# Kernel optimization log

Hardware: AMD Instinct MI355X
Metric: run time of the kernel (lower is better)

Reference implementation:

```python
import jax, jax.numpy as jnp
import numpy as np

EPS_LN = 1e-3
EPS_ATTN = 1e-8
D = 256       # slot_dim == feature_dim (required by the torch code)
H_MLP = 512
NUM_ITERS = 3  # step == 0 -> num_initial_iterations
SCALE = D ** (-0.5)


def _layernorm(x, g, b):
    m = jnp.mean(x, axis=-1, keepdims=True)
    v = jnp.mean(jnp.square(x - m), axis=-1, keepdims=True)
    return (x - m) * jax.lax.rsqrt(v + EPS_LN) * g + b


def _gru_cell(x, h, W_ih, b_ih, W_hh, b_hh):
    # torch GRUCell: W_ih [3D, D], W_hh [3D, D], gate order r, z, n
    gi = x @ W_ih.T + b_ih
    gh = h @ W_hh.T + b_hh
    i_r, i_z, i_n = jnp.split(gi, 3, axis=-1)
    h_r, h_z, h_n = jnp.split(gh, 3, axis=-1)
    r = jax.nn.sigmoid(i_r + h_r)
    z = jax.nn.sigmoid(i_z + h_z)
    n = jnp.tanh(i_n + r * h_n)
    return (1.0 - z) * n + z * h


def setup_inputs() -> dict:
    key = jax.random.key(0)
    ks = jax.random.split(key, 16)
    s = 0.02
    inp = {
        "inputs": jax.random.normal(ks[0], (32, 4096, D), jnp.float32),
        "slots": jax.random.normal(ks[1], (32, 8, D), jnp.float32),
        "step": 0,
        "ln_in_g": jnp.ones((D,), jnp.float32),
        "ln_in_b": jnp.zeros((D,), jnp.float32),
        "ln_slot_g": jnp.ones((D,), jnp.float32),
        "ln_slot_b": jnp.zeros((D,), jnp.float32),
        "ln_mlp_g": jnp.ones((D,), jnp.float32),
        "ln_mlp_b": jnp.zeros((D,), jnp.float32),
        "Wq": jax.random.normal(ks[2], (D, D), jnp.float32) * s,
        "bq": jnp.zeros((D,), jnp.float32),
        "Wk": jax.random.normal(ks[3], (D, D), jnp.float32) * s,
        "bk": jnp.zeros((D,), jnp.float32),
        "Wv": jax.random.normal(ks[4], (D, D), jnp.float32) * s,
        "bv": jnp.zeros((D,), jnp.float32),
        "W_ih": jax.random.normal(ks[5], (3 * D, D), jnp.float32) * s,
        "b_ih": jnp.zeros((3 * D,), jnp.float32),
        "W_hh": jax.random.normal(ks[6], (3 * D, D), jnp.float32) * s,
        "b_hh": jnp.zeros((3 * D,), jnp.float32),
        "W1": jax.random.normal(ks[7], (H_MLP, D), jnp.float32) * s,
        "b1": jnp.zeros((H_MLP,), jnp.float32),
        "W2": jax.random.normal(ks[8], (D, H_MLP), jnp.float32) * s,
        "b2": jnp.zeros((D,), jnp.float32),
    }
    return inp


def reference(inputs, slots, step, ln_in_g, ln_in_b, ln_slot_g, ln_slot_b,
              ln_mlp_g, ln_mlp_b, Wq, bq, Wk, bk, Wv, bv,
              W_ih, b_ih, W_hh, b_hh, W1, b1, W2, b2):
    B = inputs.shape[0]
    x = _layernorm(inputs, ln_in_g, ln_in_b)          # [B, N, D]
    k = x @ Wk.T + bk                                  # [B, N, D]
    v = x @ Wv.T + bv                                  # [B, N, D]
    num_iters = NUM_ITERS  # step == 0 -> num_initial_iterations
    for _ in range(num_iters):
        slots_prev = slots
        s_n = _layernorm(slots, ln_slot_g, ln_slot_b)  # [B, S, D]
        q = s_n @ Wq.T + bq                            # [B, S, D]
        dots = jnp.einsum('bid,bjd->bij', q, k) * SCALE  # [B, S, N]
        attn = jax.nn.softmax(dots, axis=1) + EPS_ATTN   # competitive over slots
        attn = attn / jnp.sum(attn, axis=-1, keepdims=True)
        updates = jnp.einsum('bij,bjd->bid', attn, v)  # [B, S, D]
        slots = _gru_cell(updates.reshape(-1, D), slots_prev.reshape(-1, D),
                          W_ih, b_ih, W_hh, b_hh).reshape(B, -1, D)
        mlp = jax.nn.relu(_layernorm(slots, ln_mlp_g, ln_mlp_b) @ W1.T + b1) @ W2.T + b2
        slots = slots + mlp
    return slots
```

## Files before the change

### kernel.cpp

```cpp
#include <hip/hip_runtime.h>
#include <stdint.h>


typedef __attribute__((ext_vector_type(8))) short bf16x8;
typedef __attribute__((ext_vector_type(4))) float f32x4;

__device__ __forceinline__ float bf2f_lo(uint32_t u) {
    union { uint32_t u; float f; } v; v.u = u << 16; return v.f;
}
__device__ __forceinline__ float bf2f_hi(uint32_t u) {
    union { uint32_t u; float f; } v; v.u = u & 0xffff0000u; return v.f;
}
__device__ __forceinline__ unsigned short f2bf(float f) {
    union { float f; uint32_t u; } v; v.f = f;
    return (unsigned short)((v.u + 0x7fffu + ((v.u >> 16) & 1u)) >> 16);
}
__device__ __forceinline__ float sigf(float x) { return 1.0f / (1.0f + __expf(-x)); }
__device__ __forceinline__ void gld_lds16(const void* g, void* l) {
    __builtin_amdgcn_global_load_lds(
        (__attribute__((address_space(1))) unsigned int*)g,
        (__attribute__((address_space(3))) unsigned int*)l, 16, 0, 0);
}

__global__ __launch_bounds__(256) void prep_k(
    const float* __restrict__ in, const float* __restrict__ ln_in_g,
    const float* __restrict__ ln_in_b, unsigned short* __restrict__ xbf,
    const float* __restrict__ Wk, const float* __restrict__ Wv,
    const float* __restrict__ W_ih, const float* __restrict__ W_hh,
    const float* __restrict__ W1, const float* __restrict__ W2,
    const float* __restrict__ bk, const float* __restrict__ bv,
    const float* __restrict__ b_ih, const float* __restrict__ b_hh,
    unsigned short* __restrict__ Wkv, unsigned short* __restrict__ Wg,
    unsigned short* __restrict__ W1b, unsigned short* __restrict__ W2b,
    unsigned short* __restrict__ Wqb,
    float* __restrict__ bkv, float* __restrict__ bg,
    const float* __restrict__ slots_in, const float* __restrict__ g_slot,
    const float* __restrict__ b_slot, const float* __restrict__ Wq,
    const float* __restrict__ bq, unsigned short* __restrict__ qbuf) {
    __shared__ __align__(16) char smem[16384];
    int bid = blockIdx.x, t = threadIdx.x;
    int wave = t >> 6, lane = t & 63;

    if (bid >= 3360) {
        float (*xs)[256] = (float(*)[256])smem;
        size_t rb = (size_t)(bid - 3360) * 16 + wave * 4;
        const float* gsrc = in + rb * 256;
#pragma unroll
        for (int i = 0; i < 4; ++i)
            gld_lds16(gsrc + i * 256 + lane * 4, &xs[wave * 4 + i][0]);
        __syncthreads();

        float4 g4 = *(const float4*)(ln_in_g + lane * 4);
        float4 b4 = *(const float4*)(ln_in_b + lane * 4);
#pragma unroll
        for (int p = 0; p < 2; ++p) {
            float4 x0 = *(const float4*)&xs[wave * 4 + p * 2 + 0][lane * 4];
            float4 x1 = *(const float4*)&xs[wave * 4 + p * 2 + 1][lane * 4];
            float s0 = x0.x + x0.y + x0.z + x0.w;
            float q0 = x0.x * x0.x + x0.y * x0.y + x0.z * x0.z + x0.w * x0.w;
            float s1 = x1.x + x1.y + x1.z + x1.w;
            float q1 = x1.x * x1.x + x1.y * x1.y + x1.z * x1.z + x1.w * x1.w;
#pragma unroll
            for (int off = 32; off > 0; off >>= 1) {
                s0 += __shfl_xor(s0, off, 64);  q0 += __shfl_xor(q0, off, 64);
                s1 += __shfl_xor(s1, off, 64);  q1 += __shfl_xor(q1, off, 64);
            }
            float m0 = s0 * (1.0f / 256.0f);
            float r0 = rsqrtf(q0 * (1.0f / 256.0f) - m0 * m0 + 1e-3f);
            float m1 = s1 * (1.0f / 256.0f);
            float r1 = rsqrtf(q1 * (1.0f / 256.0f) - m1 * m1 + 1e-3f);
            uint2 o0, o1;
            o0.x = (uint32_t)f2bf((x0.x - m0) * r0 * g4.x + b4.x) |
                   ((uint32_t)f2bf((x0.y - m0) * r0 * g4.y + b4.y) << 16);
            o0.y = (uint32_t)f2bf((x0.z - m0) * r0 * g4.z + b4.z) |
                   ((uint32_t)f2bf((x0.w - m0) * r0 * g4.w + b4.w) << 16);
            o1.x = (uint32_t)f2bf((x1.x - m1) * r1 * g4.x + b4.x) |
                   ((uint32_t)f2bf((x1.y - m1) * r1 * g4.y + b4.y) << 16);
            o1.y = (uint32_t)f2bf((x1.z - m1) * r1 * g4.z + b4.z) |
                   ((uint32_t)f2bf((x1.w - m1) * r1 * g4.w + b4.w) << 16);
            *(uint2*)(xbf + (rb + p * 2 + 0) * 256 + lane * 4) = o0;
            *(uint2*)(xbf + (rb + p * 2 + 1) * 256 + lane * 4) = o1;
        }
        return;
    }
    if (bid >= 32) {
        int i = (bid - 32) * 256 + t;
        if (i < 131072) {
            float v = (i < 65536) ? Wk[i] : Wv[i - 65536];
            Wkv[i] = f2bf(v);
        } else if (i < 524288) {
            int j = i - 131072;
            Wg[j] = f2bf(j < 196608 ? W_ih[j] : W_hh[j - 196608]);
        } else if (i < 655360) W1b[i - 524288] = f2bf(W1[i - 524288]);
        else if (i < 786432)   W2b[i - 655360] = f2bf(W2[i - 655360]);
        else                   Wqb[i - 786432] = f2bf(Wq[i - 786432]);
        if (i < 512)           bkv[i] = (i < 256 ? bk[i] : bv[i - 256]);
        else if (i < 2048)   { int j = i - 512; bg[j] = (j < 768 ? b_ih[j] : b_hh[j - 768]); }
        return;
    }
    int b = bid;
    unsigned short* A1 = (unsigned short*)smem;
    {
        float4 g4 = *(const float4*)(g_slot + lane * 4);
        float4 b4 = *(const float4*)(b_slot + lane * 4);
#pragma unroll
        for (int rep = 0; rep < 2; ++rep) {
            int s = wave * 2 + rep;
            float4 x = *(const float4*)(slots_in + (size_t)b * 2048 + s * 256 + lane * 4);
            float sm = x.x + x.y + x.z + x.w;
            float sq = x.x * x.x + x.y * x.y + x.z * x.z + x.w * x.w;
#pragma unroll
            for (int off = 32; off > 0; off >>= 1) {
                sm += __shfl_xor(sm, off, 64);
                sq += __shfl_xor(sq, off, 64);
            }
            float mean = sm * (1.0f / 256.0f);
            float rstd = rsqrtf(sq * (1.0f / 256.0f) - mean * mean + 1e-3f);
            uint2 o;
            o.x = (uint32_t)f2bf((x.x - mean) * rstd * g4.x + b4.x) |
                  ((uint32_t)f2bf((x.y - mean) * rstd * g4.y + b4.y) << 16);
            o.y = (uint32_t)f2bf((x.z - mean) * rstd * g4.z + b4.z) |
                  ((uint32_t)f2bf((x.w - mean) * rstd * g4.w + b4.w) << 16);
            *(uint2*)&A1[s * 264 + lane * 4] = o;
        }
    }
    __syncthreads();
    {
        bf16x8 af[8];
#pragma unroll
        for (int ks = 0; ks < 8; ++ks)
            af[ks] = *(const bf16x8*)&A1[(lane & 15) * 264 + ks * 32 + (lane >> 4) * 8];
#pragma unroll
        for (int nt = 0; nt < 4; ++nt) {
            int n0 = (wave * 4 + nt) * 16;
            f32x4 a = {0.f, 0.f, 0.f, 0.f};
#pragma unroll
            for (int ks = 0; ks < 8; ++ks) {
                const float* wp = Wq + (size_t)(n0 + (lane & 15)) * 256 +
                                  ks * 32 + (lane >> 4) * 8;
                float4 wa = *(const float4*)wp;
                float4 wb = *(const float4*)(wp + 4);
                bf16x8 bfr;
                bfr[0] = (short)f2bf(wa.x); bfr[1] = (short)f2bf(wa.y);
                bfr[2] = (short)f2bf(wa.z); bfr[3] = (short)f2bf(wa.w);
                bfr[4] = (short)f2bf(wb.x); bfr[5] = (short)f2bf(wb.y);
                bfr[6] = (short)f2bf(wb.z); bfr[7] = (short)f2bf(wb.w);
                a = __builtin_amdgcn_mfma_f32_16x16x32_bf16(af[ks], bfr, a, 0, 0, 0);
            }
            int col = n0 + (lane & 15);
            float bs = bq[col];
#pragma unroll
            for (int r = 0; r < 4; ++r) {
                int row = (lane >> 4) * 4 + r;
                if (row < 8)
                    qbuf[((size_t)b * 8 + row) * 256 + col] = f2bf(a[r] + bs);
            }
        }
    }
}

__global__ __launch_bounds__(256) void gemm_kv(const unsigned short* __restrict__ X,
                                               const unsigned short* __restrict__ W,
                                               const float* __restrict__ bkv,
                                               unsigned short* __restrict__ Ko,
                                               unsigned short* __restrict__ Vo) {
    __shared__ __align__(16) unsigned short As[128 * 64];
    __shared__ __align__(16) unsigned short Bs[128 * 64];
    int t = threadIdx.x, wave = t >> 6, lane = t & 63;
    int wr = wave >> 1, wc = wave & 1;
    int bid = blockIdx.x;
    int m0 = (((bid >> 5) << 3) | (bid & 7)) * 128;
    int j0 = ((bid >> 3) & 3) * 128;

    int rsub = lane >> 3;
    int sblk = (lane & 7) ^ rsub;

    f32x4 acc[4][4];
#pragma unroll
    for (int i = 0; i < 4; ++i)
#pragma unroll
        for (int j = 0; j < 4; ++j)
#pragma unroll
            for (int r = 0; r < 4; ++r) acc[i][j][r] = 0.f;

    for (int kb = 0; kb < 4; ++kb) {
        int k0 = kb * 64;
#pragma unroll
        for (int i = 0; i < 4; ++i) {
            int rbase = wave * 32 + i * 8;
            gld_lds16(X + (size_t)(m0 + rbase + rsub) * 256 + k0 + sblk * 8,
                      &As[rbase * 64]);
            gld_lds16(W + (size_t)(j0 + rbase + rsub) * 256 + k0 + sblk * 8,
                      &Bs[rbase * 64]);
        }
        __syncthreads();
#pragma unroll
        for (int kk = 0; kk < 64; kk += 32) {
            int koff = kk + (lane >> 4) * 8;
            int cl = koff >> 3;
            bf16x8 af[4], bf[4];
#pragma unroll
            for (int ti = 0; ti < 4; ++ti) {
                int r = wr * 64 + ti * 16 + (lane & 15);
                af[ti] = *(const bf16x8*)&As[r * 64 + ((cl ^ (r & 7)) << 3)];
            }
#pragma unroll
            for (int tj = 0; tj < 4; ++tj) {
                int c = wc * 64 + tj * 16 + (lane & 15);
                bf[tj] = *(const bf16x8*)&Bs[c * 64 + ((cl ^ (c & 7)) << 3)];
            }
#pragma unroll
            for (int ti = 0; ti < 4; ++ti)
#pragma unroll
                for (int tj = 0; tj < 4; ++tj)
                    acc[ti][tj] = __builtin_amdgcn_mfma_f32_16x16x32_bf16(
                        af[ti], bf[tj], acc[ti][tj], 0, 0, 0);
        }
        __syncthreads();
    }
    bool isK = (j0 < 256);
    unsigned short* base = isK ? Ko : Vo;
#pragma unroll
    for (int ti = 0; ti < 4; ++ti)
#pragma unroll
        for (int tj = 0; tj < 4; ++tj) {
            int col = j0 + wc * 64 + tj * 16 + (lane & 15);
            float bias = bkv[col];
            int outc = col & 255;
#pragma unroll
            for (int r = 0; r < 4; ++r) {
                int row = m0 + wr * 64 + ti * 16 + (lane >> 4) * 4 + r;
                base[(size_t)row * 256 + outc] = f2bf(acc[ti][tj][r] + bias);
            }
        }
}

__global__ __launch_bounds__(256) void attn_fused(
    const unsigned short* __restrict__ qb, const unsigned short* __restrict__ K,
    const unsigned short* __restrict__ V,
    float* __restrict__ upd_part, float* __restrict__ sums_part) {
    __shared__ __align__(16) unsigned short qs[8 * 264];
    __shared__ __align__(16) float atf[8 * 256];
    __shared__ __align__(16) float pr[4][8 * 256];
    __shared__ float ssum[8];
    int b = blockIdx.x, ch = blockIdx.y, t = threadIdx.x;
    int wave = t >> 6, lane = t & 63;

    *(uint4*)&qs[(t >> 5) * 264 + (t & 31) * 8] = ((const uint4*)(qb + (size_t)b * 2048))[t];
    if (t < 8) ssum[t] = 0.f;
    __syncthreads();

    {
        bf16x8 af[8];
#pragma unroll
        for (int ks = 0; ks < 8; ++ks)
            af[ks] = *(const bf16x8*)&qs[(lane & 7) * 264 + ks * 32 + (lane >> 4) * 8];
        const unsigned short* kb_ = K + ((size_t)b * 4096 + ch * 256) * 256;
#pragma unroll
        for (int nt = 0; nt < 4; ++nt) {
            int n0 = (wave * 4 + nt) * 16;
            const unsigned short* kp = kb_ + (size_t)(n0 + (lane & 15)) * 256 + (lane >> 4) * 8;
            f32x4 a = {0.f, 0.f, 0.f, 0.f};
#pragma unroll
            for (int ks = 0; ks < 8; ++ks) {
                bf16x8 bfr = *(const bf16x8*)(kp + ks * 32);
                a = __builtin_amdgcn_mfma_f32_16x16x32_bf16(af[ks], bfr, a, 0, 0, 0);
            }
            if (lane < 32) {
                int n = n0 + (lane & 15);
                int s0 = (lane >> 4) * 4;
#pragma unroll
                for (int r = 0; r < 4; ++r)
                    atf[(s0 + r) * 256 + n] = a[r] * 0.0625f;
            }
        }
    }
    __syncthreads();

    {
        int n = t;
        float v[8];
#pragma unroll
        for (int s = 0; s < 8; ++s) v[s] = atf[s * 256 + n];
        float m = v[0];
#pragma unroll
        for (int s = 1; s < 8; ++s) m = fmaxf(m, v[s]);
        float sum = 0.f;
#pragma unroll
        for (int s = 0; s < 8; ++s) { v[s] = __expf(v[s] - m); sum += v[s]; }
        float inv = 1.0f / sum;
        float ts[8];
#pragma unroll
        for (int s = 0; s < 8; ++s) {
            float a = v[s] * inv + 1e-8f;
            atf[s * 256 + n] = a;
            ts[s] = a;
        }
#pragma unroll
        for (int s = 0; s < 8; ++s) {
#pragma unroll
            for (int off = 32; off > 0; off >>= 1)
                ts[s] += __shfl_xor(ts[s], off, 64);
        }
        if (lane == 0) {
#pragma unroll
            for (int s = 0; s < 8; ++s) atomicAdd(&ssum[s], ts[s]);
        }
    }
    __syncthreads();
    if (t < 8) sums_part[((size_t)ch * 32 + b) * 8 + t] = ssum[t];

    float ua[8][4];
#pragma unroll
    for (int s = 0; s < 8; ++s)
#pragma unroll
        for (int k = 0; k < 4; ++k) ua[s][k] = 0.f;
    const unsigned short* vb = V + ((size_t)b * 4096 + ch * 256 + wave * 64) * 256 + lane * 4;
    uint2 vv[4], vn[4];
#pragma unroll
    for (int kk = 0; kk < 4; ++kk) vv[kk] = *(const uint2*)(vb + (size_t)kk * 256);
    for (int g = 0; g < 16; ++g) {
        if (g < 15) {
            const unsigned short* nrow = vb + (size_t)(g + 1) * 1024;
#pragma unroll
            for (int kk = 0; kk < 4; ++kk) vn[kk] = *(const uint2*)(nrow + (size_t)kk * 256);
        }
        int nl = wave * 64 + g * 4;
        float4 a4[8];
#pragma unroll
        for (int s = 0; s < 8; ++s) a4[s] = *(const float4*)&atf[s * 256 + nl];
#define UPD_STEP(kk, comp)                                                     \
        {                                                                      \
            float v0 = bf2f_lo(vv[kk].x), v1 = bf2f_hi(vv[kk].x);              \
            float v2 = bf2f_lo(vv[kk].y), v3 = bf2f_hi(vv[kk].y);              \
            _Pragma("unroll")                                                  \
            for (int s = 0; s < 8; ++s) {                                      \
                float a = a4[s].comp;                                          \
                ua[s][0] += a * v0; ua[s][1] += a * v1;                        \
                ua[s][2] += a * v2; ua[s][3] += a * v3;                        \
            }                                                                  \
        }
        UPD_STEP(0, x) UPD_STEP(1, y) UPD_STEP(2, z) UPD_STEP(3, w)
#undef UPD_STEP
#pragma unroll
        for (int kk = 0; kk < 4; ++kk) vv[kk] = vn[kk];
    }
#pragma unroll
    for (int s = 0; s < 8; ++s)
        *(float4*)&pr[wave][s * 256 + lane * 4] = *(float4*)ua[s];
    __syncthreads();
    float* updp = upd_part + ((size_t)ch * 32 + b) * 2048;
    for (int i = t; i < 2048; i += 256)
        updp[i] = pr[0][i] + pr[1][i] + pr[2][i] + pr[3][i];
}

__global__ __launch_bounds__(512, 1) void slot_tail(
    const float* __restrict__ upd_part, const float* __restrict__ sums_part,
    const float* __restrict__ cur,
    const unsigned short* __restrict__ Wg, const float* __restrict__ bg,
    const float* __restrict__ g_mlp, const float* __restrict__ b_mlp,
    const unsigned short* __restrict__ W1b, const float* __restrict__ b1,
    const unsigned short* __restrict__ W2b, const float* __restrict__ b2,
    const float* __restrict__ g_slot, const float* __restrict__ b_slot,
    const unsigned short* __restrict__ Wqb, const float* __restrict__ bq,
    float* __restrict__ slots_out, unsigned short* __restrict__ qbuf,
    int do_q) {
    __shared__ float gts[8 * 1536];
    __shared__ float hn[2048];
    __shared__ float sn[2048];
    __shared__ __align__(16) unsigned short A1u[8 * 264];
    __shared__ __align__(16) unsigned short A1h[8 * 264];
    __shared__ __align__(16) unsigned short A1[8 * 264];
    __shared__ __align__(16) unsigned short A2[8 * 520];
    __shared__ float ssum8[8];
    int b = blockIdx.x, t = threadIdx.x;
    int wave = t >> 6, lane = t & 63;

    if (t < 8) {
        float s8 = 0.f;
#pragma unroll
        for (int c = 0; c < 16; ++c) s8 += sums_part[((size_t)c * 32 + b) * 8 + t];
        ssum8[t] = s8;
    }
    __syncthreads();
    for (int idx = t; idx < 2048; idx += 512) {
        float us = 0.f;
#pragma unroll
        for (int c = 0; c < 16; ++c) us += upd_part[((size_t)c * 32 + b) * 2048 + idx];
        int row = idx >> 8, d = idx & 255;
        A1u[row * 264 + d] = f2bf(us / ssum8[row]);
        A1h[row * 264 + d] = f2bf(cur[(size_t)b * 2048 + idx]);
    }
    __syncthreads();

    {
        const unsigned short* Af = (wave < 4) ? A1u : A1h;
        bf16x8 af[8];
#pragma unroll
        for (int ks = 0; ks < 8; ++ks)
            af[ks] = *(const bf16x8*)&Af[(lane & 15) * 264 + ks * 32 + (lane >> 4) * 8];
#pragma unroll
        for (int nt = 0; nt < 12; ++nt) {
            int n0 = wave * 192 + nt * 16;
            f32x4 a = {0.f, 0.f, 0.f, 0.f};
#pragma unroll
            for (int ks = 0; ks < 8; ++ks) {
                bf16x8 bfr = *(const bf16x8*)(Wg + (size_t)(n0 + (lane & 15)) * 256 +
                                              ks * 32 + (lane >> 4) * 8);
                a = __builtin_amdgcn_mfma_f32_16x16x32_bf16(af[ks], bfr, a, 0, 0, 0);
            }
            int col = n0 + (lane & 15);
            float bs = bg[col];
#pragma unroll
            for (int r = 0; r < 4; ++r) {
                int row = (lane >> 4) * 4 + r;
                if (row < 8) gts[row * 1536 + col] = a[r] + bs;
            }
        }
    }
    __syncthreads();

#pragma unroll
    for (int p = 0; p < 4; ++p) {
        int idx = p * 512 + t;
        int s = idx >> 8, j = idx & 255;
        const float* gr = &gts[s * 1536];
        float r  = sigf(gr[j] + gr[768 + j]);
        float z  = sigf(gr[256 + j] + gr[1024 + j]);
        float nn = tanhf(gr[512 + j] + r * gr[1280 + j]);
        float h  = cur[(size_t)b * 2048 + idx];
        hn[idx] = (1.0f - z) * nn + z * h;
    }
    __syncthreads();

    {
        float4 g4 = *(const float4*)(g_mlp + lane * 4);
        float4 b4 = *(const float4*)(b_mlp + lane * 4);
        int s = wave;
        float4 x = *(const float4*)&hn[s * 256 + lane * 4];
        float sm = x.x + x.y + x.z + x.w;
        float sq = x.x * x.x + x.y * x.y + x.z * x.z + x.w * x.w;
#pragma unroll
        for (int off = 32; off > 0; off >>= 1) {
            sm += __shfl_xor(sm, off, 64);
            sq += __shfl_xor(sq, off, 64);
        }
        float mean = sm * (1.0f / 256.0f);
        float rstd = rsqrtf(sq * (1.0f / 256.0f) - mean * mean + 1e-3f);
        uint2 o;
        o.x = (uint32_t)f2bf((x.x - mean) * rstd * g4.x + b4.x) |
              ((uint32_t)f2bf((x.y - mean) * rstd * g4.y + b4.y) << 16);
        o.y = (uint32_t)f2bf((x.z - mean) * rstd * g4.z + b4.z) |
              ((uint32_t)f2bf((x.w - mean) * rstd * g4.w + b4.w) << 16);
        *(uint2*)&A1[s * 264 + lane * 4] = o;
    }
    __syncthreads();

    {
        bf16x8 af[8];
#pragma unroll
        for (int ks = 0; ks < 8; ++ks)
            af[ks] = *(const bf16x8*)&A1[(lane & 15) * 264 + ks * 32 + (lane >> 4) * 8];
#pragma unroll
        for (int nt = 0; nt < 4; ++nt) {
            int n0 = (wave * 4 + nt) * 16;
            f32x4 a = {0.f, 0.f, 0.f, 0.f};
#pragma unroll
            for (int ks = 0; ks < 8; ++ks) {
                bf16x8 bfr = *(const bf16x8*)(W1b + (size_t)(n0 + (lane & 15)) * 256 +
                                              ks * 32 + (lane >> 4) * 8);
                a = __builtin_amdgcn_mfma_f32_16x16x32_bf16(af[ks], bfr, a, 0, 0, 0);
            }
            int col = n0 + (lane & 15);
            float bs = b1[col];
#pragma unroll
            for (int r = 0; r < 4; ++r) {
                int row = (lane >> 4) * 4 + r;
                if (row < 8) A2[row * 520 + col] = f2bf(fmaxf(a[r] + bs, 0.f));
            }
        }
    }
    __syncthreads();

    {
        bf16x8 af[16];
#pragma unroll
        for (int ks = 0; ks < 16; ++ks)
            af[ks] = *(const bf16x8*)&A2[(lane & 15) * 520 + ks * 32 + (lane >> 4) * 8];
#pragma unroll
        for (int nt = 0; nt < 2; ++nt) {
            int n0 = (wave * 2 + nt) * 16;
            f32x4 a = {0.f, 0.f, 0.f, 0.f};
#pragma unroll
            for (int ks = 0; ks < 16; ++ks) {
                bf16x8 bfr = *(const bf16x8*)(W2b + (size_t)(n0 + (lane & 15)) * 512 +
                                              ks * 32 + (lane >> 4) * 8);
                a = __builtin_amdgcn_mfma_f32_16x16x32_bf16(af[ks], bfr, a, 0, 0, 0);
            }
            int col = n0 + (lane & 15);
            float bs = b2[col];
#pragma unroll
            for (int r = 0; r < 4; ++r) {
                int row = (lane >> 4) * 4 + r;
                if (row < 8) {
                    float v = a[r] + bs + hn[row * 256 + col];
                    sn[row * 256 + col] = v;
                    slots_out[((size_t)b * 8 + row) * 256 + col] = v;
                }
            }
        }
    }
    if (!do_q) return;
    __syncthreads();

    {
        float4 g4 = *(const float4*)(g_slot + lane * 4);
        float4 b4 = *(const float4*)(b_slot + lane * 4);
        int s = wave;
        float4 x = *(const float4*)&sn[s * 256 + lane * 4];
        float sm = x.x + x.y + x.z + x.w;
        float sq = x.x * x.x + x.y * x.y + x.z * x.z + x.w * x.w;
#pragma unroll
        for (int off = 32; off > 0; off >>= 1) {
            sm += __shfl_xor(sm, off, 64);
            sq += __shfl_xor(sq, off, 64);
        }
        float mean = sm * (1.0f / 256.0f);
        float rstd = rsqrtf(sq * (1.0f / 256.0f) - mean * mean + 1e-3f);
        uint2 o;
        o.x = (uint32_t)f2bf((x.x - mean) * rstd * g4.x + b4.x) |
              ((uint32_t)f2bf((x.y - mean) * rstd * g4.y + b4.y) << 16);
        o.y = (uint32_t)f2bf((x.z - mean) * rstd * g4.z + b4.z) |
              ((uint32_t)f2bf((x.w - mean) * rstd * g4.w + b4.w) << 16);
        *(uint2*)&A1[s * 264 + lane * 4] = o;
    }
    __syncthreads();

    {
        bf16x8 af[8];
#pragma unroll
        for (int ks = 0; ks < 8; ++ks)
            af[ks] = *(const bf16x8*)&A1[(lane & 15) * 264 + ks * 32 + (lane >> 4) * 8];
#pragma unroll
        for (int nt = 0; nt < 2; ++nt) {
            int n0 = (wave * 2 + nt) * 16;
            f32x4 a = {0.f, 0.f, 0.f, 0.f};
#pragma unroll
            for (int ks = 0; ks < 8; ++ks) {
                bf16x8 bfr = *(const bf16x8*)(Wqb + (size_t)(n0 + (lane & 15)) * 256 +
                                              ks * 32 + (lane >> 4) * 8);
                a = __builtin_amdgcn_mfma_f32_16x16x32_bf16(af[ks], bfr, a, 0, 0, 0);
            }
            int col = n0 + (lane & 15);
            float bs = bq[col];
#pragma unroll
            for (int r = 0; r < 4; ++r) {
                int row = (lane >> 4) * 4 + r;
                if (row < 8)
                    qbuf[((size_t)b * 8 + row) * 256 + col] = f2bf(a[r] + bs);
            }
        }
    }
}

extern "C" void kernel_launch(void* const* d_in, const int* in_sizes, int n_in,
                              void* d_out, int out_size, void* d_ws, size_t ws_size,
                              hipStream_t stream) {
    const float* inputs    = (const float*)d_in[0];
    const float* slots_in  = (const float*)d_in[1];
    const float* ln_in_g   = (const float*)d_in[3];
    const float* ln_in_b   = (const float*)d_in[4];
    const float* ln_slot_g = (const float*)d_in[5];
    const float* ln_slot_b = (const float*)d_in[6];
    const float* ln_mlp_g  = (const float*)d_in[7];
    const float* ln_mlp_b  = (const float*)d_in[8];
    const float* Wq   = (const float*)d_in[9];
    const float* bq   = (const float*)d_in[10];
    const float* Wk   = (const float*)d_in[11];
    const float* bk   = (const float*)d_in[12];
    const float* Wv   = (const float*)d_in[13];
    const float* bv   = (const float*)d_in[14];
    const float* W_ih = (const float*)d_in[15];
    const float* b_ih = (const float*)d_in[16];
    const float* W_hh = (const float*)d_in[17];
    const float* b_hh = (const float*)d_in[18];
    const float* W1   = (const float*)d_in[19];
    const float* b1   = (const float*)d_in[20];
    const float* W2   = (const float*)d_in[21];
    const float* b2   = (const float*)d_in[22];

    char* p = (char*)d_ws;
    size_t off = 0;
    auto take = [&](size_t bytes) -> char* {
        char* r = p + off;
        off += (bytes + 255) & ~(size_t)255;
        return r;
    };
    unsigned short* xbf  = (unsigned short*)take((size_t)131072 * 256 * 2);
    unsigned short* Kb   = (unsigned short*)take((size_t)131072 * 256 * 2);
    unsigned short* Vb   = (unsigned short*)take((size_t)131072 * 256 * 2);
    unsigned short* Wkv  = (unsigned short*)take(131072 * 2);
    unsigned short* Wg   = (unsigned short*)take(393216 * 2);
    unsigned short* W1b  = (unsigned short*)take(131072 * 2);
    unsigned short* W2b  = (unsigned short*)take(131072 * 2);
    unsigned short* Wqb  = (unsigned short*)take(65536 * 2);
    float* bkv   = (float*)take(512 * 4);
    float* bg    = (float*)take(1536 * 4);
    unsigned short* qbuf = (unsigned short*)take(65536 * 2);
    float* upd_part  = (float*)take((size_t)16 * 32 * 2048 * 4);
    float* sums_part = (float*)take((size_t)16 * 32 * 8 * 4);
    float* sA    = (float*)take(65536 * 4);
    float* sB    = (float*)take(65536 * 4);

    prep_k<<<11552, 256, 0, stream>>>(inputs, ln_in_g, ln_in_b, xbf,
                                      Wk, Wv, W_ih, W_hh, W1, W2,
                                      bk, bv, b_ih, b_hh,
                                      Wkv, Wg, W1b, W2b, Wqb, bkv, bg,
                                      slots_in, ln_slot_g, ln_slot_b, Wq, bq, qbuf);
    gemm_kv<<<4096, 256, 0, stream>>>(xbf, Wkv, bkv, Kb, Vb);

    const float* cur = slots_in;
    float* nxt[3] = {sA, sB, (float*)d_out};
    for (int it = 0; it < 3; ++it) {
        attn_fused<<<dim3(32, 16), 256, 0, stream>>>(qbuf, Kb, Vb, upd_part, sums_part);
        slot_tail<<<32, 512, 0, stream>>>(upd_part, sums_part, cur, Wg, bg,
                                          ln_mlp_g, ln_mlp_b, W1b, b1, W2b, b2,
                                          ln_slot_g, ln_slot_b, Wqb, bq,
                                          nxt[it], qbuf, it < 2 ? 1 : 0);
        cur = nxt[it];
    }
    (void)in_sizes; (void)n_in; (void)out_size; (void)ws_size;
}
```

Measured before the change: 515.9 us.

## Split attention into 32 token chunks per batch and reduce partials via LDS atomics

```diff
diff --git a/kernel.cpp b/kernel.cpp
--- a/kernel.cpp
+++ b/kernel.cpp
@@ -240,14 +240,16 @@
     const unsigned short* __restrict__ V,
     float* __restrict__ upd_part, float* __restrict__ sums_part) {
     __shared__ __align__(16) unsigned short qs[8 * 264];
-    __shared__ __align__(16) float atf[8 * 256];
-    __shared__ __align__(16) float pr[4][8 * 256];
+    __shared__ __align__(16) float atf[8 * 128];
+    __shared__ __align__(16) float upd_lds[8 * 256];
     __shared__ float ssum[8];
     int b = blockIdx.x, ch = blockIdx.y, t = threadIdx.x;
     int wave = t >> 6, lane = t & 63;
 
     *(uint4*)&qs[(t >> 5) * 264 + (t & 31) * 8] = ((const uint4*)(qb + (size_t)b * 2048))[t];
     if (t < 8) ssum[t] = 0.f;
+#pragma unroll
+    for (int i = 0; i < 8; ++i) upd_lds[i * 256 + t] = 0.f;
     __syncthreads();
 
     {
@@ -255,10 +257,10 @@
 #pragma unroll
         for (int ks = 0; ks < 8; ++ks)
             af[ks] = *(const bf16x8*)&qs[(lane & 7) * 264 + ks * 32 + (lane >> 4) * 8];
-        const unsigned short* kb_ = K + ((size_t)b * 4096 + ch * 256) * 256;
-#pragma unroll
-        for (int nt = 0; nt < 4; ++nt) {
-            int n0 = (wave * 4 + nt) * 16;
+        const unsigned short* kb_ = K + ((size_t)b * 4096 + ch * 128) * 256;
+#pragma unroll
+        for (int nt = 0; nt < 2; ++nt) {
+            int n0 = (wave * 2 + nt) * 16;
             const unsigned short* kp = kb_ + (size_t)(n0 + (lane & 15)) * 256 + (lane >> 4) * 8;
             f32x4 a = {0.f, 0.f, 0.f, 0.f};
 #pragma unroll
@@ -271,17 +273,17 @@
                 int s0 = (lane >> 4) * 4;
 #pragma unroll
                 for (int r = 0; r < 4; ++r)
-                    atf[(s0 + r) * 256 + n] = a[r] * 0.0625f;
-            }
-        }
-    }
-    __syncthreads();
-
-    {
+                    atf[(s0 + r) * 128 + n] = a[r] * 0.0625f;
+            }
+        }
+    }
+    __syncthreads();
+
+    if (t < 128) {
         int n = t;
         float v[8];
 #pragma unroll
-        for (int s = 0; s < 8; ++s) v[s] = atf[s * 256 + n];
+        for (int s = 0; s < 8; ++s) v[s] = atf[s * 128 + n];
         float m = v[0];
 #pragma unroll
         for (int s = 1; s < 8; ++s) m = fmaxf(m, v[s]);
@@ -293,7 +295,7 @@
 #pragma unroll
         for (int s = 0; s < 8; ++s) {
             float a = v[s] * inv + 1e-8f;
-            atf[s * 256 + n] = a;
+            atf[s * 128 + n] = a;
             ts[s] = a;
         }
 #pragma unroll
@@ -315,20 +317,20 @@
     for (int s = 0; s < 8; ++s)
 #pragma unroll
         for (int k = 0; k < 4; ++k) ua[s][k] = 0.f;
-    const unsigned short* vb = V + ((size_t)b * 4096 + ch * 256 + wave * 64) * 256 + lane * 4;
+    const unsigned short* vb = V + ((size_t)b * 4096 + ch * 128 + wave * 32) * 256 + lane * 4;
     uint2 vv[4], vn[4];
 #pragma unroll
     for (int kk = 0; kk < 4; ++kk) vv[kk] = *(const uint2*)(vb + (size_t)kk * 256);
-    for (int g = 0; g < 16; ++g) {
-        if (g < 15) {
+    for (int g = 0; g < 8; ++g) {
+        if (g < 7) {
             const unsigned short* nrow = vb + (size_t)(g + 1) * 1024;
 #pragma unroll
             for (int kk = 0; kk < 4; ++kk) vn[kk] = *(const uint2*)(nrow + (size_t)kk * 256);
         }
-        int nl = wave * 64 + g * 4;
+        int nl = wave * 32 + g * 4;
         float4 a4[8];
 #pragma unroll
-        for (int s = 0; s < 8; ++s) a4[s] = *(const float4*)&atf[s * 256 + nl];
+        for (int s = 0; s < 8; ++s) a4[s] = *(const float4*)&atf[s * 128 + nl];
 #define UPD_STEP(kk, comp)                                                     \
         {                                                                      \
             float v0 = bf2f_lo(vv[kk].x), v1 = bf2f_hi(vv[kk].x);              \
@@ -347,11 +349,12 @@
     }
 #pragma unroll
     for (int s = 0; s < 8; ++s)
-        *(float4*)&pr[wave][s * 256 + lane * 4] = *(float4*)ua[s];
+#pragma unroll
+        for (int k = 0; k < 4; ++k)
+            atomicAdd(&upd_lds[s * 256 + lane * 4 + k], ua[s][k]);
     __syncthreads();
     float* updp = upd_part + ((size_t)ch * 32 + b) * 2048;
-    for (int i = t; i < 2048; i += 256)
-        updp[i] = pr[0][i] + pr[1][i] + pr[2][i] + pr[3][i];
+    for (int i = t; i < 2048; i += 256) updp[i] = upd_lds[i];
 }
 
 __global__ __launch_bounds__(512, 1) void slot_tail(
@@ -379,17 +382,29 @@
     if (t < 8) {
         float s8 = 0.f;
 #pragma unroll
-        for (int c = 0; c < 16; ++c) s8 += sums_part[((size_t)c * 32 + b) * 8 + t];
+        for (int c = 0; c < 32; ++c) s8 += sums_part[((size_t)c * 32 + b) * 8 + t];
         ssum8[t] = s8;
     }
     __syncthreads();
-    for (int idx = t; idx < 2048; idx += 512) {
-        float us = 0.f;
-#pragma unroll
-        for (int c = 0; c < 16; ++c) us += upd_part[((size_t)c * 32 + b) * 2048 + idx];
+    {
+        int idx = t * 4;
+        float4 us = make_float4(0.f, 0.f, 0.f, 0.f);
+#pragma unroll
+        for (int c = 0; c < 32; ++c) {
+            float4 v = *(const float4*)&upd_part[((size_t)c * 32 + b) * 2048 + idx];
+            us.x += v.x; us.y += v.y; us.z += v.z; us.w += v.w;
+        }
         int row = idx >> 8, d = idx & 255;
-        A1u[row * 264 + d] = f2bf(us / ssum8[row]);
-        A1h[row * 264 + d] = f2bf(cur[(size_t)b * 2048 + idx]);
+        float inv = 1.0f / ssum8[row];
+        uint2 o;
+        o.x = (uint32_t)f2bf(us.x * inv) | ((uint32_t)f2bf(us.y * inv) << 16);
+        o.y = (uint32_t)f2bf(us.z * inv) | ((uint32_t)f2bf(us.w * inv) << 16);
+        *(uint2*)&A1u[row * 264 + d] = o;
+        float4 h = *(const float4*)&cur[(size_t)b * 2048 + idx];
+        uint2 oh;
+        oh.x = (uint32_t)f2bf(h.x) | ((uint32_t)f2bf(h.y) << 16);
+        oh.y = (uint32_t)f2bf(h.z) | ((uint32_t)f2bf(h.w) << 16);
+        *(uint2*)&A1h[row * 264 + d] = oh;
     }
     __syncthreads();
 
@@ -607,8 +622,8 @@
     float* bkv   = (float*)take(512 * 4);
     float* bg    = (float*)take(1536 * 4);
     unsigned short* qbuf = (unsigned short*)take(65536 * 2);
-    float* upd_part  = (float*)take((size_t)16 * 32 * 2048 * 4);
-    float* sums_part = (float*)take((size_t)16 * 32 * 8 * 4);
+    float* upd_part  = (float*)take((size_t)32 * 32 * 2048 * 4);
+    float* sums_part = (float*)take((size_t)32 * 32 * 8 * 4);
     float* sA    = (float*)take(65536 * 4);
     float* sB    = (float*)take(65536 * 4);
 
@@ -622,7 +637,7 @@
     const float* cur = slots_in;
     float* nxt[3] = {sA, sB, (float*)d_out};
     for (int it = 0; it < 3; ++it) {
-        attn_fused<<<dim3(32, 16), 256, 0, stream>>>(qbuf, Kb, Vb, upd_part, sums_part);
+        attn_fused<<<dim3(32, 32), 256, 0, stream>>>(qbuf, Kb, Vb, upd_part, sums_part);
         slot_tail<<<32, 512, 0, stream>>>(upd_part, sums_part, cur, Wg, bg,
                                           ln_mlp_g, ln_mlp_b, W1b, b1, W2b, b2,
                                           ln_slot_g, ln_slot_b, Wqb, bq,
```

After: 644.8 us. +25.0%, slower.
